# Performance work log

Hardware: AMD Instinct MI355X
Metric: run time of the kernel (lower is better)

## Reference

```python
import jax, jax.numpy as jnp
import numpy as np

L, NH, DH, D, DI, V = 12, 12, 64, 768, 3072, 10000
QLEN, MLEN, CLEN, BSZ = 512, 512, 32, 4
EPS = 1e-5


def _ln(x, g, b):
    m = x.mean(-1, keepdims=True)
    v = ((x - m) ** 2).mean(-1, keepdims=True)
    return (x - m) / jnp.sqrt(v + EPS) * g + b


def _rel_shift(x):
    # x: [B, H, qlen, rlen]; Transformer-XL pad/reshape shift trick
    B, H, q, r = x.shape
    xp = jnp.pad(x, ((0, 0), (0, 0), (0, 0), (1, 0)))
    return xp.reshape(B, H, r + 1, q)[:, :, 1:, :].reshape(B, H, q, r)


def _pos_emb(klen):
    # positions klen-1 .. 0 (relative distances), sinusoidal, dim D
    pos = jnp.arange(klen - 1, -1, -1, dtype=jnp.float32)
    inv = 1.0 / (10000.0 ** (jnp.arange(0, D, 2, dtype=jnp.float32) / D))
    s = pos[:, None] * inv[None, :]
    return jnp.concatenate([jnp.sin(s), jnp.cos(s)], axis=-1)  # [klen, D]


def setup_inputs() -> dict:
    key = jax.random.key(0)
    ks = jax.random.split(key, 21)
    init = lambda k, shape: (0.02 * jax.random.normal(k, shape)).astype(jnp.float32)
    return {
        'x': jax.random.randint(ks[0], (QLEN, BSZ), 0, V),
        'condition': init(ks[1], (CLEN, BSZ, D)) * 50.0,
        'mems': init(ks[2], (L, MLEN, BSZ, D)) * 50.0,
        'emb': init(ks[3], (V, D)),
        'qkv_w': init(ks[4], (L, D, 3 * NH * DH)),
        'r_net_w': init(ks[5], (L, D, NH * DH)),
        'o_w': init(ks[6], (L, NH * DH, D)),
        'ln1_g': jnp.ones((L, D), jnp.float32),
        'ln1_b': jnp.zeros((L, D), jnp.float32),
        'w1': init(ks[7], (L, D, DI)),
        'b1': jnp.zeros((L, DI), jnp.float32),
        'w2': init(ks[8], (L, DI, D)),
        'b2': jnp.zeros((L, D), jnp.float32),
        'ln2_g': jnp.ones((L, D), jnp.float32),
        'ln2_b': jnp.zeros((L, D), jnp.float32),
        'r_w_bias': init(ks[9], (NH, DH)),
        'r_r_bias': init(ks[10], (NH, DH)),
        'proj_w': init(ks[11], (D, V)),
        'proj_b': jnp.zeros((V,), jnp.float32),
    }


def reference(x, condition, mems, emb, qkv_w, r_net_w, o_w, ln1_g, ln1_b,
              w1, b1, w2, b2, ln2_g, ln2_b, r_w_bias, r_r_bias, proj_w, proj_b):
    qlen, bsz = x.shape
    klen = CLEN + MLEN + qlen
    h = emb[x] * jnp.sqrt(jnp.float32(D))  # [qlen, B, D] word emb * sqrt(d_model)
    r = _pos_emb(klen)                      # [klen, D]
    scale = 1.0 / jnp.sqrt(jnp.float32(DH))
    # causal mask: query i may attend to keys j <= CLEN + MLEN + i (True = masked)
    mask = jnp.arange(klen)[None, :] > (jnp.arange(qlen)[:, None] + CLEN + MLEN)
    for l in range(L):
        cat = jnp.concatenate([condition, mems[l], h], axis=0)  # [klen, B, D]
        heads = cat @ qkv_w[l]                                   # [klen, B, 3*NH*DH]
        qh, kh, vh = jnp.split(heads, 3, axis=-1)
        qh = qh[-qlen:].reshape(qlen, bsz, NH, DH)
        kh = kh.reshape(klen, bsz, NH, DH)
        vh = vh.reshape(klen, bsz, NH, DH)
        rk = (r @ r_net_w[l]).reshape(klen, NH, DH)
        AC = jnp.einsum('ibnd,jbnd->bnij', qh + r_w_bias, kh)    # content score
        BD = _rel_shift(jnp.einsum('ibnd,jnd->bnij', qh + r_r_bias, rk))  # position score
        score = (AC + BD) * scale
        score = jnp.where(mask[None, None], -jnp.inf, score)
        prob = jax.nn.softmax(score, axis=-1)
        av = jnp.einsum('bnij,jbnd->ibnd', prob, vh).reshape(qlen, bsz, NH * DH)
        h = _ln(h + av @ o_w[l], ln1_g[l], ln1_b[l])             # post-LN attention
        ff = jax.nn.relu(h @ w1[l] + b1[l]) @ w2[l] + b2[l]
        h = _ln(h + ff, ln2_g[l], ln2_b[l])                      # post-LN FFN
    return h @ proj_w + proj_b  # [qlen, B, n_token] logits
```

## Files before the change

### kernel.cpp

```cpp
#include <hip/hip_runtime.h>
#include <stdint.h>

#define NLAYER 12
#define NH 12
#define DH 64
#define DMODEL 768
#define DI 3072
#define NV 10000
#define QLEN 512
#define MLEN 512
#define CLEN 32
#define BSZ 4
#define KLEN (CLEN + MLEN + QLEN)
#define MQ (QLEN * BSZ)
#define MK (KLEN * BSZ)
#define H3 (3 * NH * DH)
#define HD (NH * DH)
#define NG (BSZ * NH)
#define SROW ((size_t)QLEN * KLEN)
#define KPAD_R 1152
#define NPAD_V 10112
#define NGC 24

typedef __bf16 bf16;
typedef __bf16 bf16x8 __attribute__((ext_vector_type(8)));
typedef float f32x4 __attribute__((ext_vector_type(4)));

__device__ __forceinline__ void gload16(const void* g, void* l) {
    __builtin_amdgcn_global_load_lds((const __attribute__((address_space(1))) void*)g,
                                     (__attribute__((address_space(3))) void*)l, 16, 0, 0);
}

__device__ __forceinline__ void split_store(float x, bf16* __restrict__ hp,
                                            bf16* __restrict__ lp, size_t off) {
    bf16 h = (bf16)x;
    hp[off] = h;
    lp[off] = (bf16)(x - (float)h);
}

__device__ __forceinline__ void raster(int& bx, int& by) {
    int gx = gridDim.x, gy = gridDim.y;
    int nwg = gx * gy;
    int wgid = blockIdx.y * gx + blockIdx.x;
    int q = nwg >> 3, r = nwg & 7;
    int xcd = wgid & 7, lin = wgid >> 3;
    int swz = (xcd < r ? xcd * (q + 1) : r * (q + 1) + (xcd - r) * q) + lin;
    int gsz = gx * 4;
    int grp = swz / gsz, rem = swz % gsz;
    int rows = gy - grp * 4;
    if (rows > 4) rows = 4;
    bx = rem / rows;
    by = grp * 4 + rem % rows;
}

__global__ __launch_bounds__(256) void k_embed(const int* __restrict__ x,
                                               const float* __restrict__ emb,
                                               float* __restrict__ h) {
    int idx = blockIdx.x * 256 + threadIdx.x;
    if (idx >= MQ * DMODEL) return;
    int row = idx / DMODEL;
    int d = idx % DMODEL;
    int tok = x[row];
    h[idx] = emb[(size_t)tok * DMODEL + d] * 27.712812921102035f;
}

__global__ __launch_bounds__(256) void k_posemb(bf16* __restrict__ rh, bf16* __restrict__ rl) {
    int idx = blockIdx.x * 256 + threadIdx.x;
    if (idx >= KPAD_R * DMODEL) return;
    int k = idx / DMODEL;
    int d = idx % DMODEL;
    float v = 0.0f;
    if (k < KLEN) {
        int pos = KLEN - 1 - k;
        int j = (d < DMODEL / 2) ? d : d - DMODEL / 2;
        double inv = exp(-((double)(2 * j) / (double)DMODEL) * log(10000.0));
        double s = (double)pos * inv;
        v = (d < DMODEL / 2) ? (float)sin(s) : (float)cos(s);
    }
    split_store(v, rh, rl, (size_t)idx);
}

__global__ __launch_bounds__(256) void k_zpad(bf16* __restrict__ khH, bf16* __restrict__ khL) {
    int idx = blockIdx.x * 256 + threadIdx.x;
    int tot = NG * (KPAD_R - KLEN) * DH;
    if (idx >= tot) return;
    int g = idx / ((KPAD_R - KLEN) * DH);
    int rem = idx % ((KPAD_R - KLEN) * DH);
    int jr = rem / DH, d = rem % DH;
    size_t off = ((size_t)g * KPAD_R + KLEN + jr) * DH + d;
    khH[off] = (bf16)0.0f;
    khL[off] = (bf16)0.0f;
}

__global__ __launch_bounds__(256) void k_concat(const float* __restrict__ cond,
                                                const float* __restrict__ mem_l,
                                                const float* __restrict__ h,
                                                bf16* __restrict__ catH,
                                                bf16* __restrict__ catL) {
    int idx = blockIdx.x * 256 + threadIdx.x;
    if (idx >= MK * DMODEL) return;
    int row = idx / DMODEL;
    int k = row / BSZ;
    float v;
    if (k < CLEN) v = cond[idx];
    else if (k < CLEN + MLEN) v = mem_l[idx - CLEN * BSZ * DMODEL];
    else v = h[idx - (CLEN + MLEN) * BSZ * DMODEL];
    split_store(v, catH, catL, (size_t)idx);
}

__global__ __launch_bounds__(256) void k_wconv(const float* __restrict__ W,
                                               bf16* __restrict__ Bh,
                                               bf16* __restrict__ Bl,
                                               int K, int N) {
    __shared__ float t[32][33];
    int n0 = blockIdx.x * 32, k0 = blockIdx.y * 32;
    int tc = threadIdx.x & 31, tr = threadIdx.x >> 5;
#pragma unroll
    for (int i = 0; i < 32; i += 8) {
        int n = n0 + tc;
        t[tr + i][tc] = (n < N) ? W[(size_t)(k0 + tr + i) * N + n] : 0.0f;
    }
    __syncthreads();
#pragma unroll
    for (int i = 0; i < 32; i += 8) {
        int n = n0 + tr + i;
        int k = k0 + tc;
        float x = t[tc][tr + i];
        size_t off = (size_t)n * K + k;
        bf16 h = (bf16)x;
        Bh[off] = h;
        Bl[off] = (bf16)(x - (float)h);
    }
}

template <int BM, bool BIAS, bool RELU, bool SPLITOUT, int SK>
__global__ __launch_bounds__(256) void k_mgemm(const bf16* __restrict__ Ahi,
                                               const bf16* __restrict__ Alo,
                                               const bf16* __restrict__ Bhi,
                                               const bf16* __restrict__ Blo,
                                               const float* __restrict__ bias,
                                               float* __restrict__ C,
                                               bf16* __restrict__ Chi,
                                               bf16* __restrict__ Clo,
                                               int M, int N, int K, int ldc) {
    constexpr int MI = (BM == 128) ? 4 : 2;
    __shared__ __align__(16) bf16 As[2][BM][32];
    __shared__ __align__(16) bf16 Bs[2][128][32];
    int bx, by;
    raster(bx, by);
    int z = (SK > 1) ? blockIdx.z : 0;
    int kb = K / SK;
    int kbeg = z * kb, kend = kbeg + kb;
    if (SK > 1) C += (size_t)z * M * ldc;
    int tid = threadIdx.x;
    int lane = tid & 63;
    int wave = tid >> 6;
    int bm = by * BM, bn = bx * 128;
    int wr = (wave >> 1) * (BM / 2), wc = (wave & 1) * 64;
    int fr = lane & 15;
    int fk = (lane >> 4) * 8;

    const f32x4 fzero = {0.f, 0.f, 0.f, 0.f};
    f32x4 acc[MI][4];
#pragma unroll
    for (int i = 0; i < MI; i++)
#pragma unroll
        for (int j = 0; j < 4; j++) acc[i][j] = fzero;

    int r0 = tid >> 2, p0 = (tid & 3) * 8;
    int r1 = r0 + 64, p1 = p0;

    for (int k0 = kbeg; k0 < kend; k0 += 32) {
        if (BM == 128) {
            gload16(Ahi + (size_t)(bm + r0) * K + k0 + p0, &As[0][r0][p0]);
            gload16(Ahi + (size_t)(bm + r1) * K + k0 + p1, &As[0][r1 & (BM - 1)][p1]);
            gload16(Alo + (size_t)(bm + r0) * K + k0 + p0, &As[1][r0][p0]);
            gload16(Alo + (size_t)(bm + r1) * K + k0 + p1, &As[1][r1 & (BM - 1)][p1]);
        } else {
            gload16(Ahi + (size_t)(bm + r0) * K + k0 + p0, &As[0][r0 & (BM - 1)][p0]);
            gload16(Alo + (size_t)(bm + r0) * K + k0 + p0, &As[1][r0 & (BM - 1)][p0]);
        }
        gload16(Bhi + (size_t)(bn + r0) * K + k0 + p0, &Bs[0][r0][p0]);
        gload16(Bhi + (size_t)(bn + r1) * K + k0 + p1, &Bs[0][r1][p1]);
        gload16(Blo + (size_t)(bn + r0) * K + k0 + p0, &Bs[1][r0][p0]);
        gload16(Blo + (size_t)(bn + r1) * K + k0 + p1, &Bs[1][r1][p1]);
        __syncthreads();

        bf16x8 ah[MI], al[MI], bh[4], bl[4];
#pragma unroll
        for (int mi = 0; mi < MI; mi++) {
            ah[mi] = *(const bf16x8*)&As[0][wr + mi * 16 + fr][fk];
            al[mi] = *(const bf16x8*)&As[1][wr + mi * 16 + fr][fk];
        }
#pragma unroll
        for (int ni = 0; ni < 4; ni++) {
            bh[ni] = *(const bf16x8*)&Bs[0][wc + ni * 16 + fr][fk];
            bl[ni] = *(const bf16x8*)&Bs[1][wc + ni * 16 + fr][fk];
        }
#pragma unroll
        for (int mi = 0; mi < MI; mi++)
#pragma unroll
            for (int ni = 0; ni < 4; ni++) {
                acc[mi][ni] = __builtin_amdgcn_mfma_f32_16x16x32_bf16(ah[mi], bh[ni], acc[mi][ni], 0, 0, 0);
                acc[mi][ni] = __builtin_amdgcn_mfma_f32_16x16x32_bf16(ah[mi], bl[ni], acc[mi][ni], 0, 0, 0);
                acc[mi][ni] = __builtin_amdgcn_mfma_f32_16x16x32_bf16(al[mi], bh[ni], acc[mi][ni], 0, 0, 0);
            }
        __syncthreads();
    }

#pragma unroll
    for (int mi = 0; mi < MI; mi++) {
        int rowb = bm + wr + mi * 16 + (lane >> 4) * 4;
#pragma unroll
        for (int ni = 0; ni < 4; ni++) {
            int col = bn + wc + ni * 16 + fr;
            if (col >= N) continue;
            float bv = (BIAS && z == 0) ? bias[col] : 0.0f;
#pragma unroll
            for (int r = 0; r < 4; r++) {
                int row = rowb + r;
                if (row >= M) continue;
                float xv = acc[mi][ni][r] + bv;
                if (RELU) xv = fmaxf(xv, 0.0f);
                size_t off = (size_t)row * ldc + col;
                if (SPLITOUT) {
                    bf16 hh = (bf16)xv;
                    Chi[off] = hh;
                    Clo[off] = (bf16)(xv - (float)hh);
                } else {
                    C[off] = xv;
                }
            }
        }
    }
}

template <int MODE>
__global__ __launch_bounds__(256) void k_mgemm_qkv(const bf16* __restrict__ Ahi,
                                                   const bf16* __restrict__ Alo,
                                                   const bf16* __restrict__ Bhi,
                                                   const bf16* __restrict__ Blo,
                                                   const float* __restrict__ rwb,
                                                   const float* __restrict__ rrb,
                                                   bf16* __restrict__ P0H, bf16* __restrict__ P0L,
                                                   bf16* __restrict__ P1H, bf16* __restrict__ P1L) {
    constexpr int K = DMODEL;
    __shared__ __align__(16) bf16 As[2][128][32];
    __shared__ __align__(16) bf16 Bs[2][128][32];
    int bx, by;
    raster(bx, by);
    int tid = threadIdx.x;
    int lane = tid & 63;
    int wave = tid >> 6;
    int bm = by * 128, bn = bx * 128;
    int wr = (wave >> 1) * 64, wc = (wave & 1) * 64;
    int fr = lane & 15;
    int fk = (lane >> 4) * 8;

    const f32x4 fzero = {0.f, 0.f, 0.f, 0.f};
    f32x4 acc[4][4];
#pragma unroll
    for (int i = 0; i < 4; i++)
#pragma unroll
        for (int j = 0; j < 4; j++) acc[i][j] = fzero;

    int r0 = tid >> 2, p0 = (tid & 3) * 8;
    int r1 = r0 + 64, p1 = p0;

    for (int k0 = 0; k0 < K; k0 += 32) {
        gload16(Ahi + (size_t)(bm + r0) * K + k0 + p0, &As[0][r0][p0]);
        gload16(Ahi + (size_t)(bm + r1) * K + k0 + p1, &As[0][r1][p1]);
        gload16(Alo + (size_t)(bm + r0) * K + k0 + p0, &As[1][r0][p0]);
        gload16(Alo + (size_t)(bm + r1) * K + k0 + p1, &As[1][r1][p1]);
        gload16(Bhi + (size_t)(bn + r0) * K + k0 + p0, &Bs[0][r0][p0]);
        gload16(Bhi + (size_t)(bn + r1) * K + k0 + p1, &Bs[0][r1][p1]);
        gload16(Blo + (size_t)(bn + r0) * K + k0 + p0, &Bs[1][r0][p0]);
        gload16(Blo + (size_t)(bn + r1) * K + k0 + p1, &Bs[1][r1][p1]);
        __syncthreads();

        bf16x8 ah[4], al[4], bh[4], bl[4];
#pragma unroll
        for (int mi = 0; mi < 4; mi++) {
            ah[mi] = *(const bf16x8*)&As[0][wr + mi * 16 + fr][fk];
            al[mi] = *(const bf16x8*)&As[1][wr + mi * 16 + fr][fk];
        }
#pragma unroll
        for (int ni = 0; ni < 4; ni++) {
            bh[ni] = *(const bf16x8*)&Bs[0][wc + ni * 16 + fr][fk];
            bl[ni] = *(const bf16x8*)&Bs[1][wc + ni * 16 + fr][fk];
        }
#pragma unroll
        for (int mi = 0; mi < 4; mi++)
#pragma unroll
            for (int ni = 0; ni < 4; ni++) {
                acc[mi][ni] = __builtin_amdgcn_mfma_f32_16x16x32_bf16(ah[mi], bh[ni], acc[mi][ni], 0, 0, 0);
                acc[mi][ni] = __builtin_amdgcn_mfma_f32_16x16x32_bf16(ah[mi], bl[ni], acc[mi][ni], 0, 0, 0);
                acc[mi][ni] = __builtin_amdgcn_mfma_f32_16x16x32_bf16(al[mi], bh[ni], acc[mi][ni], 0, 0, 0);
            }
        __syncthreads();
    }

#pragma unroll
    for (int mi = 0; mi < 4; mi++) {
        int rowb = bm + wr + mi * 16 + (lane >> 4) * 4;
#pragma unroll
        for (int ni = 0; ni < 4; ni++) {
            int col = bn + wc + ni * 16 + fr;
#pragma unroll
            for (int r = 0; r < 4; r++) {
                int row = rowb + r;
                float xv = acc[mi][ni][r];
                int b = row & 3;
                if (MODE == 0) {
                    int i = row >> 2;
                    int g = b * NH + (col >> 6);
                    int d = col & 63;
                    size_t off = ((size_t)g * QLEN + i) * DH + d;
                    split_store((xv + rwb[col]) * 0.125f, P0H, P0L, off);
                    split_store((xv + rrb[col]) * 0.125f, P1H, P1L, off);
                } else {
                    int j = row >> 2;
                    if (col < HD) {
                        int g = b * NH + (col >> 6);
                        int d = col & 63;
                        split_store(xv, P0H, P0L, ((size_t)g * KPAD_R + j) * DH + d);
                    } else {
                        int c2 = col - HD;
                        int g = b * NH + (c2 >> 6);
                        int d = c2 & 63;
                        split_store(xv, P1H, P1L, ((size_t)g * KLEN + j) * DH + d);
                    }
                }
            }
        }
    }
}

__global__ __launch_bounds__(256) void k_vtconv_b(const bf16* __restrict__ vH,
                                                  const bf16* __restrict__ vL,
                                                  bf16* __restrict__ vtH,
                                                  bf16* __restrict__ vtL,
                                                  int g0) {
    __shared__ bf16 th[32][33], tl[32][33];
    int gl = blockIdx.z;
    int g = g0 + gl;
    int j0 = blockIdx.x * 32, d0 = blockIdx.y * 32;
    int tc = threadIdx.x & 31, tr = threadIdx.x >> 5;
#pragma unroll
    for (int i = 0; i < 32; i += 8) {
        size_t src = ((size_t)g * KLEN + j0 + tr + i) * DH + d0 + tc;
        th[tr + i][tc] = vH[src];
        tl[tr + i][tc] = vL[src];
    }
    __syncthreads();
#pragma unroll
    for (int i = 0; i < 32; i += 8) {
        size_t dst = ((size_t)gl * DH + d0 + tr + i) * KLEN + j0 + tc;
        vtH[dst] = th[tc][tr + i];
        vtL[dst] = tl[tc][tr + i];
    }
}

template <bool SHIFT>
__global__ __launch_bounds__(256) void k_score(const bf16* __restrict__ QH,
                                               const bf16* __restrict__ QL,
                                               const bf16* __restrict__ KHp,
                                               const bf16* __restrict__ KLp,
                                               float* __restrict__ sAc,
                                               int g0) {
    int bm = blockIdx.y * 128, bn = blockIdx.x * 128;
    if (!SHIFT && bn >= bm + 672) return;
    if (SHIFT && bn + bm < 257) return;
    int gl = blockIdx.z;
    int g = g0 + gl;
    int n = g % NH;
    const bf16* Ah = QH + (size_t)g * QLEN * DH;
    const bf16* Al = QL + (size_t)g * QLEN * DH;
    const bf16 *Bh, *Bl;
    int ldb;
    if (SHIFT) { Bh = KHp + n * DH; Bl = KLp + n * DH; ldb = HD; }
    else { Bh = KHp + (size_t)g * KPAD_R * DH; Bl = KLp + (size_t)g * KPAD_R * DH; ldb = DH; }
    float* C = sAc + (size_t)gl * SROW;

    __shared__ __align__(16) bf16 As[2][128][32];
    __shared__ __align__(16) bf16 Bs[2][128][32];
    int tid = threadIdx.x;
    int lane = tid & 63;
    int wave = tid >> 6;
    int wr = (wave >> 1) * 64, wc = (wave & 1) * 64;
    int fr = lane & 15;
    int fk = (lane >> 4) * 8;

    const f32x4 fzero = {0.f, 0.f, 0.f, 0.f};
    f32x4 acc[4][4];
#pragma unroll
    for (int i = 0; i < 4; i++)
#pragma unroll
        for (int j = 0; j < 4; j++) acc[i][j] = fzero;

    int r0 = tid >> 2, p0 = (tid & 3) * 8;
    int r1 = r0 + 64, p1 = p0;

#pragma unroll
    for (int k0 = 0; k0 < DH; k0 += 32) {
        gload16(Ah + (size_t)(bm + r0) * DH + k0 + p0, &As[0][r0][p0]);
        gload16(Ah + (size_t)(bm + r1) * DH + k0 + p1, &As[0][r1][p1]);
        gload16(Al + (size_t)(bm + r0) * DH + k0 + p0, &As[1][r0][p0]);
        gload16(Al + (size_t)(bm + r1) * DH + k0 + p1, &As[1][r1][p1]);
        gload16(Bh + (size_t)(bn + r0) * ldb + k0 + p0, &Bs[0][r0][p0]);
        gload16(Bh + (size_t)(bn + r1) * ldb + k0 + p1, &Bs[0][r1][p1]);
        gload16(Bl + (size_t)(bn + r0) * ldb + k0 + p0, &Bs[1][r0][p0]);
        gload16(Bl + (size_t)(bn + r1) * ldb + k0 + p1, &Bs[1][r1][p1]);
        __syncthreads();

        bf16x8 ah[4], al[4], bh[4], bl[4];
#pragma unroll
        for (int mi = 0; mi < 4; mi++) {
            ah[mi] = *(const bf16x8*)&As[0][wr + mi * 16 + fr][fk];
            al[mi] = *(const bf16x8*)&As[1][wr + mi * 16 + fr][fk];
        }
#pragma unroll
        for (int ni = 0; ni < 4; ni++) {
            bh[ni] = *(const bf16x8*)&Bs[0][wc + ni * 16 + fr][fk];
            bl[ni] = *(const bf16x8*)&Bs[1][wc + ni * 16 + fr][fk];
        }
#pragma unroll
        for (int mi = 0; mi < 4; mi++)
#pragma unroll
            for (int ni = 0; ni < 4; ni++) {
                acc[mi][ni] = __builtin_amdgcn_mfma_f32_16x16x32_bf16(ah[mi], bh[ni], acc[mi][ni], 0, 0, 0);
                acc[mi][ni] = __builtin_amdgcn_mfma_f32_16x16x32_bf16(ah[mi], bl[ni], acc[mi][ni], 0, 0, 0);
                acc[mi][ni] = __builtin_amdgcn_mfma_f32_16x16x32_bf16(al[mi], bh[ni], acc[mi][ni], 0, 0, 0);
            }
        __syncthreads();
    }

#pragma unroll
    for (int mi = 0; mi < 4; mi++) {
        int rowb = bm + wr + mi * 16 + (lane >> 4) * 4;
#pragma unroll
        for (int ni = 0; ni < 4; ni++) {
            int t = bn + wc + ni * 16 + fr;
            if (t >= KLEN) continue;
#pragma unroll
            for (int r = 0; r < 4; r++) {
                int i = rowb + r;
                if (SHIFT) {
                    int j = t - (QLEN - 1) + i;
                    if (j >= 0) C[(size_t)i * KLEN + j] += acc[mi][ni][r];
                } else {
                    C[(size_t)i * KLEN + t] = acc[mi][ni][r];
                }
            }
        }
    }
}

__global__ __launch_bounds__(256) void k_softmax_p(const float* __restrict__ sAc,
                                                   bf16* __restrict__ P) {
    __shared__ float red[256];
    int i = blockIdx.x;
    int gl = blockIdx.y;
    int tid = threadIdx.x;
    const float* row = sAc + (size_t)gl * SROW + (size_t)i * KLEN;
    bf16* pr = P + (size_t)gl * SROW + (size_t)i * KLEN;
    int len = i + CLEN + MLEN + 1;
    float v[5];
    int cnt = 0;
    float mx = -1e30f;
    for (int j = tid; j < len; j += 256) {
        float s = row[j];
        v[cnt++] = s;
        mx = fmaxf(mx, s);
    }
    red[tid] = mx;
    __syncthreads();
    for (int st = 128; st > 0; st >>= 1) {
        if (tid < st) red[tid] = fmaxf(red[tid], red[tid + st]);
        __syncthreads();
    }
    float smax = red[0];
    __syncthreads();
    float sum = 0.f;
    cnt = 0;
    for (int j = tid; j < len; j += 256) {
        float e = __expf(v[cnt] - smax);
        v[cnt] = e;
        sum += e;
        cnt++;
    }
    red[tid] = sum;
    __syncthreads();
    for (int st = 128; st > 0; st >>= 1) {
        if (tid < st) red[tid] += red[tid + st];
        __syncthreads();
    }
    float inv = 1.0f / red[0];
    cnt = 0;
    for (int j = tid; j < len; j += 256) pr[j] = (bf16)(v[cnt++] * inv);
    for (int j = tid; j < KLEN; j += 256)
        if (j >= len) pr[j] = (bf16)0.0f;
}

__global__ __launch_bounds__(256) void k_av(const bf16* __restrict__ P,
                                            const bf16* __restrict__ VH,
                                            const bf16* __restrict__ VL,
                                            bf16* __restrict__ atH,
                                            bf16* __restrict__ atL,
                                            int g0) {
    int gl = blockIdx.z;
    int g = g0 + gl;
    int b = g / NH, n = g % NH;
    const bf16* Ap = P + (size_t)gl * SROW;
    const bf16* Vh = VH + (size_t)gl * DH * KLEN;
    const bf16* Vl = VL + (size_t)gl * DH * KLEN;
    __shared__ __align__(16) bf16 As[64][32];
    __shared__ __align__(16) bf16 Bs[2][64][32];
    int tid = threadIdx.x;
    int lane = tid & 63;
    int wave = tid >> 6;
    int bm = blockIdx.y * 64;
    int fr = lane & 15;
    int fk = (lane >> 4) * 8;
    const f32x4 fzero = {0.f, 0.f, 0.f, 0.f};
    f32x4 acc[4] = {fzero, fzero, fzero, fzero};
    int ra = tid >> 2, pa = (tid & 3) * 8;
    int kmax = bm + 608;
    if (kmax > KLEN) kmax = KLEN;

    for (int k0 = 0; k0 < kmax; k0 += 32) {
        gload16(Ap + (size_t)(bm + ra) * KLEN + k0 + pa, &As[ra][pa]);
        gload16(Vh + (size_t)ra * KLEN + k0 + pa, &Bs[0][ra][pa]);
        gload16(Vl + (size_t)ra * KLEN + k0 + pa, &Bs[1][ra][pa]);
        __syncthreads();
        bf16x8 a = *(const bf16x8*)&As[wave * 16 + fr][fk];
#pragma unroll
        for (int ni = 0; ni < 4; ni++) {
            bf16x8 bh = *(const bf16x8*)&Bs[0][ni * 16 + fr][fk];
            bf16x8 bl = *(const bf16x8*)&Bs[1][ni * 16 + fr][fk];
            acc[ni] = __builtin_amdgcn_mfma_f32_16x16x32_bf16(a, bh, acc[ni], 0, 0, 0);
            acc[ni] = __builtin_amdgcn_mfma_f32_16x16x32_bf16(a, bl, acc[ni], 0, 0, 0);
        }
        __syncthreads();
    }

#pragma unroll
    for (int ni = 0; ni < 4; ni++) {
        int d = ni * 16 + fr;
#pragma unroll
        for (int r = 0; r < 4; r++) {
            int i = bm + wave * 16 + (lane >> 4) * 4 + r;
            size_t off = (size_t)(i * BSZ + b) * HD + n * DH + d;
            split_store(acc[ni][r], atH, atL, off);
        }
    }
}

__global__ __launch_bounds__(256) void k_add_ln(float* __restrict__ h,
                                                const float* __restrict__ d0,
                                                const float* __restrict__ d1,
                                                const float* __restrict__ g,
                                                const float* __restrict__ bta,
                                                bf16* __restrict__ hH,
                                                bf16* __restrict__ hL) {
    __shared__ float xs[DMODEL];
    __shared__ float red[256];
    int row = blockIdx.x;
    int tid = threadIdx.x;
    float* hr = h + (size_t)row * DMODEL;
    const float* dr0 = d0 + (size_t)row * DMODEL;
    const float* dr1 = d1 + (size_t)row * DMODEL;
    float s = 0.f;
    for (int d = tid; d < DMODEL; d += 256) {
        float v = hr[d] + dr0[d] + dr1[d];
        xs[d] = v;
        s += v;
    }
    red[tid] = s;
    __syncthreads();
    for (int st = 128; st > 0; st >>= 1) {
        if (tid < st) red[tid] += red[tid + st];
        __syncthreads();
    }
    float mean = red[0] * (1.0f / DMODEL);
    __syncthreads();
    float v2 = 0.f;
    for (int d = tid; d < DMODEL; d += 256) {
        float t = xs[d] - mean;
        v2 += t * t;
    }
    red[tid] = v2;
    __syncthreads();
    for (int st = 128; st > 0; st >>= 1) {
        if (tid < st) red[tid] += red[tid + st];
        __syncthreads();
    }
    float inv = rsqrtf(red[0] * (1.0f / DMODEL) + 1e-5f);
    for (int d = tid; d < DMODEL; d += 256) {
        float y = (xs[d] - mean) * inv * g[d] + bta[d];
        hr[d] = y;
        split_store(y, hH, hL, (size_t)row * DMODEL + d);
    }
}

extern "C" void kernel_launch(void* const* d_in, const int* in_sizes, int n_in,
                              void* d_out, int out_size, void* d_ws, size_t ws_size,
                              hipStream_t stream) {
    const int* x = (const int*)d_in[0];
    const float* condition = (const float*)d_in[1];
    const float* mems = (const float*)d_in[2];
    const float* emb = (const float*)d_in[3];
    const float* qkv_w = (const float*)d_in[4];
    const float* r_net_w = (const float*)d_in[5];
    const float* o_w = (const float*)d_in[6];
    const float* ln1_g = (const float*)d_in[7];
    const float* ln1_b = (const float*)d_in[8];
    const float* w1 = (const float*)d_in[9];
    const float* b1 = (const float*)d_in[10];
    const float* w2 = (const float*)d_in[11];
    const float* b2 = (const float*)d_in[12];
    const float* ln2_g = (const float*)d_in[13];
    const float* ln2_b = (const float*)d_in[14];
    const float* r_w_bias = (const float*)d_in[15];
    const float* r_r_bias = (const float*)d_in[16];
    const float* proj_w = (const float*)d_in[17];
    const float* proj_b = (const float*)d_in[18];
    float* out = (float*)d_out;

    float* ws = (float*)d_ws;
    float* h = ws;
    float* delta = h + (size_t)MQ * DMODEL;
    float* delta2 = delta + (size_t)MQ * DMODEL;

    bf16* pb = (bf16*)(delta2 + (size_t)MQ * DMODEL);
    bf16* rbH = pb; pb += (size_t)KPAD_R * DMODEL;
    bf16* rbL = pb; pb += (size_t)KPAD_R * DMODEL;
    bf16* rkH = pb; pb += (size_t)KPAD_R * DMODEL;
    bf16* rkL = pb; pb += (size_t)KPAD_R * DMODEL;
    bf16* atH = pb; pb += (size_t)MQ * HD;
    bf16* atL = pb; pb += (size_t)MQ * HD;
    bf16* qwH = pb; pb += (size_t)NG * QLEN * DH;
    bf16* qwL = pb; pb += (size_t)NG * QLEN * DH;
    bf16* qrH = pb; pb += (size_t)NG * QLEN * DH;
    bf16* qrL = pb; pb += (size_t)NG * QLEN * DH;
    bf16* khH = pb; pb += (size_t)NG * KPAD_R * DH;
    bf16* khL = pb; pb += (size_t)NG * KPAD_R * DH;
    bf16* vH_ = pb; pb += (size_t)NG * KLEN * DH;
    bf16* vL_ = pb; pb += (size_t)NG * KLEN * DH;

    bf16* R = pb;
    bf16* BtH = R;
    bf16* BtL = BtH + (size_t)NPAD_V * DMODEL;
    bf16* ffnH = BtL + (size_t)NPAD_V * DMODEL;
    bf16* ffnL = ffnH + (size_t)MQ * DI;
    bf16* catH = ffnL + (size_t)MQ * DI;
    bf16* catL = catH + (size_t)MK * DMODEL;
    bf16* hH = catL + (size_t)MK * DMODEL;
    bf16* hL = hH + (size_t)MQ * DMODEL;

    float* sAc = (float*)R;
    bf16* Pc = (bf16*)(sAc + (size_t)NGC * SROW);
    bf16* vtH = Pc + (size_t)NGC * SROW;
    bf16* vtL = vtH + (size_t)NGC * DH * KLEN;

    dim3 blk(256);
    k_embed<<<dim3((MQ * DMODEL + 255) / 256), blk, 0, stream>>>(x, emb, h);
    k_posemb<<<dim3((KPAD_R * DMODEL + 255) / 256), blk, 0, stream>>>(rbH, rbL);
    k_zpad<<<dim3((NG * (KPAD_R - KLEN) * DH + 255) / 256), blk, 0, stream>>>(khH, khL);

    for (int l = 0; l < NLAYER; l++) {
        k_concat<<<dim3((MK * DMODEL + 255) / 256), blk, 0, stream>>>(
            condition, mems + (size_t)l * MLEN * BSZ * DMODEL, h, catH, catL);

        k_wconv<<<dim3(H3 / 32, DMODEL / 32), blk, 0, stream>>>(
            qkv_w + (size_t)l * DMODEL * H3, BtH, BtL, DMODEL, H3);
        k_mgemm_qkv<1><<<dim3((2 * HD) / 128, MK / 128), blk, 0, stream>>>(
            catH, catL, BtH + (size_t)HD * DMODEL, BtL + (size_t)HD * DMODEL,
            nullptr, nullptr, khH, khL, vH_, vL_);
        k_mgemm_qkv<0><<<dim3(HD / 128, MQ / 128), blk, 0, stream>>>(
            catH + (size_t)(CLEN + MLEN) * BSZ * DMODEL, catL + (size_t)(CLEN + MLEN) * BSZ * DMODEL,
            BtH, BtL, r_w_bias, r_r_bias, qwH, qwL, qrH, qrL);

        k_wconv<<<dim3(HD / 32, DMODEL / 32), blk, 0, stream>>>(
            r_net_w + (size_t)l * DMODEL * HD, BtH, BtL, DMODEL, HD);
        k_mgemm<64, false, false, true, 1><<<dim3(HD / 128, KPAD_R / 64), blk, 0, stream>>>(
            rbH, rbL, BtH, BtL, nullptr, nullptr, rkH, rkL, KPAD_R, HD, DMODEL, HD);

        for (int g0 = 0; g0 < NG; g0 += NGC) {
            k_vtconv_b<<<dim3(KLEN / 32, DH / 32, NGC), blk, 0, stream>>>(vH_, vL_, vtH, vtL, g0);
            k_score<false><<<dim3(KPAD_R / 128, QLEN / 128, NGC), blk, 0, stream>>>(
                qwH, qwL, khH, khL, sAc, g0);
            k_score<true><<<dim3(KPAD_R / 128, QLEN / 128, NGC), blk, 0, stream>>>(
                qrH, qrL, rkH, rkL, sAc, g0);
            k_softmax_p<<<dim3(QLEN, NGC), blk, 0, stream>>>(sAc, Pc);
            k_av<<<dim3(1, QLEN / 64, NGC), blk, 0, stream>>>(Pc, vtH, vtL, atH, atL, g0);
        }

        k_wconv<<<dim3(DMODEL / 32, HD / 32), blk, 0, stream>>>(
            o_w + (size_t)l * HD * DMODEL, BtH, BtL, HD, DMODEL);
        k_mgemm<64, false, false, false, 2><<<dim3(DMODEL / 128, MQ / 64, 2), blk, 0, stream>>>(
            atH, atL, BtH, BtL, nullptr, delta, nullptr, nullptr, MQ, DMODEL, HD, DMODEL);

        k_add_ln<<<dim3(MQ), blk, 0, stream>>>(h, delta, delta2, ln1_g + (size_t)l * DMODEL,
                                               ln1_b + (size_t)l * DMODEL, hH, hL);

        k_wconv<<<dim3(DI / 32, DMODEL / 32), blk, 0, stream>>>(
            w1 + (size_t)l * DMODEL * DI, BtH, BtL, DMODEL, DI);
        k_mgemm<128, true, true, true, 1><<<dim3(DI / 128, MQ / 128), blk, 0, stream>>>(
            hH, hL, BtH, BtL, b1 + (size_t)l * DI, nullptr, ffnH, ffnL, MQ, DI, DMODEL, DI);

        k_wconv<<<dim3(DMODEL / 32, DI / 32), blk, 0, stream>>>(
            w2 + (size_t)l * DI * DMODEL, BtH, BtL, DI, DMODEL);
        k_mgemm<64, true, false, false, 2><<<dim3(DMODEL / 128, MQ / 64, 2), blk, 0, stream>>>(
            ffnH, ffnL, BtH, BtL, b2 + (size_t)l * DMODEL, delta, nullptr, nullptr,
            MQ, DMODEL, DI, DMODEL);

        k_add_ln<<<dim3(MQ), blk, 0, stream>>>(h, delta, delta2, ln2_g + (size_t)l * DMODEL,
                                               ln2_b + (size_t)l * DMODEL, hH, hL);
    }

    k_wconv<<<dim3(NPAD_V / 32, DMODEL / 32), blk, 0, stream>>>(proj_w, BtH, BtL, DMODEL, NV);
    k_mgemm<128, true, false, false, 1><<<dim3(NPAD_V / 128, MQ / 128), blk, 0, stream>>>(
        hH, hL, BtH, BtL, proj_b, out, nullptr, nullptr, MQ, NV, DMODEL, NV);
}
```

Before: 6.509 ms.

## Fuse content score, softmax and AV into a flash-style attention kernel

Replaces the separate content-score GEMM, softmax and P·V kernels with a single online-softmax kernel that computes Q·K per tile, adds a precomputed unshifted position-score matrix read with shifted indexing, and accumulates P·V in registers. The position scores are now written unshifted, with no read-modify-write into a shared score buffer. This removes the float score round-trip and the bf16 probability matrix in global memory. In exchange it adds gathered loads of the position scores and swizzled LDS tiles, and the softmax is rescaled per tile with probabilities rounded to bf16.

```diff
diff --git a/kernel.cpp b/kernel.cpp
--- a/kernel.cpp
+++ b/kernel.cpp
@@ -361,26 +361,22 @@
     }
 }
 
-template <bool SHIFT>
-__global__ __launch_bounds__(256) void k_score(const bf16* __restrict__ QH,
-                                               const bf16* __restrict__ QL,
-                                               const bf16* __restrict__ KHp,
-                                               const bf16* __restrict__ KLp,
-                                               float* __restrict__ sAc,
-                                               int g0) {
+__global__ __launch_bounds__(256) void k_bdt(const bf16* __restrict__ QH,
+                                             const bf16* __restrict__ QL,
+                                             const bf16* __restrict__ RH,
+                                             const bf16* __restrict__ RL,
+                                             float* __restrict__ BDt,
+                                             int g0) {
     int bm = blockIdx.y * 128, bn = blockIdx.x * 128;
-    if (!SHIFT && bn >= bm + 672) return;
-    if (SHIFT && bn + bm < 257) return;
+    if (bn + bm <= 256) return;
     int gl = blockIdx.z;
     int g = g0 + gl;
     int n = g % NH;
     const bf16* Ah = QH + (size_t)g * QLEN * DH;
     const bf16* Al = QL + (size_t)g * QLEN * DH;
-    const bf16 *Bh, *Bl;
-    int ldb;
-    if (SHIFT) { Bh = KHp + n * DH; Bl = KLp + n * DH; ldb = HD; }
-    else { Bh = KHp + (size_t)g * KPAD_R * DH; Bl = KLp + (size_t)g * KPAD_R * DH; ldb = DH; }
-    float* C = sAc + (size_t)gl * SROW;
+    const bf16* Bh = RH + n * DH;
+    const bf16* Bl = RL + n * DH;
+    float* C = BDt + (size_t)gl * SROW;
 
     __shared__ __align__(16) bf16 As[2][128][32];
     __shared__ __align__(16) bf16 Bs[2][128][32];
@@ -407,10 +403,10 @@
         gload16(Ah + (size_t)(bm + r1) * DH + k0 + p1, &As[0][r1][p1]);
         gload16(Al + (size_t)(bm + r0) * DH + k0 + p0, &As[1][r0][p0]);
         gload16(Al + (size_t)(bm + r1) * DH + k0 + p1, &As[1][r1][p1]);
-        gload16(Bh + (size_t)(bn + r0) * ldb + k0 + p0, &Bs[0][r0][p0]);
-        gload16(Bh + (size_t)(bn + r1) * ldb + k0 + p1, &Bs[0][r1][p1]);
-        gload16(Bl + (size_t)(bn + r0) * ldb + k0 + p0, &Bs[1][r0][p0]);
-        gload16(Bl + (size_t)(bn + r1) * ldb + k0 + p1, &Bs[1][r1][p1]);
+        gload16(Bh + (size_t)(bn + r0) * HD + k0 + p0, &Bs[0][r0][p0]);
+        gload16(Bh + (size_t)(bn + r1) * HD + k0 + p1, &Bs[0][r1][p1]);
+        gload16(Bl + (size_t)(bn + r0) * HD + k0 + p0, &Bs[1][r0][p0]);
+        gload16(Bl + (size_t)(bn + r1) * HD + k0 + p1, &Bs[1][r1][p1]);
         __syncthreads();
 
         bf16x8 ah[4], al[4], bh[4], bl[4];
@@ -445,113 +441,186 @@
 #pragma unroll
             for (int r = 0; r < 4; r++) {
                 int i = rowb + r;
-                if (SHIFT) {
-                    int j = t - (QLEN - 1) + i;
-                    if (j >= 0) C[(size_t)i * KLEN + j] += acc[mi][ni][r];
-                } else {
-                    C[(size_t)i * KLEN + t] = acc[mi][ni][r];
-                }
-            }
-        }
-    }
-}
-
-__global__ __launch_bounds__(256) void k_softmax_p(const float* __restrict__ sAc,
-                                                   bf16* __restrict__ P) {
-    __shared__ float red[256];
-    int i = blockIdx.x;
+                C[(size_t)i * KLEN + t] = acc[mi][ni][r];
+            }
+        }
+    }
+}
+
+__global__ __launch_bounds__(256) void k_flash(const bf16* __restrict__ qwH, const bf16* __restrict__ qwL,
+                                               const bf16* __restrict__ khH, const bf16* __restrict__ khL,
+                                               const bf16* __restrict__ vtH, const bf16* __restrict__ vtL,
+                                               const float* __restrict__ BDt,
+                                               bf16* __restrict__ atH, bf16* __restrict__ atL,
+                                               int g0) {
+    __shared__ __align__(16) bf16 LQ[2][64][64];
+    __shared__ __align__(16) bf16 LK[2][64][64];
+    __shared__ __align__(16) bf16 LV[2][64][64];
+    __shared__ __align__(16) bf16 LP[64][64];
     int gl = blockIdx.y;
-    int tid = threadIdx.x;
-    const float* row = sAc + (size_t)gl * SROW + (size_t)i * KLEN;
-    bf16* pr = P + (size_t)gl * SROW + (size_t)i * KLEN;
-    int len = i + CLEN + MLEN + 1;
-    float v[5];
-    int cnt = 0;
-    float mx = -1e30f;
-    for (int j = tid; j < len; j += 256) {
-        float s = row[j];
-        v[cnt++] = s;
-        mx = fmaxf(mx, s);
-    }
-    red[tid] = mx;
-    __syncthreads();
-    for (int st = 128; st > 0; st >>= 1) {
-        if (tid < st) red[tid] = fmaxf(red[tid], red[tid + st]);
-        __syncthreads();
-    }
-    float smax = red[0];
-    __syncthreads();
-    float sum = 0.f;
-    cnt = 0;
-    for (int j = tid; j < len; j += 256) {
-        float e = __expf(v[cnt] - smax);
-        v[cnt] = e;
-        sum += e;
-        cnt++;
-    }
-    red[tid] = sum;
-    __syncthreads();
-    for (int st = 128; st > 0; st >>= 1) {
-        if (tid < st) red[tid] += red[tid + st];
-        __syncthreads();
-    }
-    float inv = 1.0f / red[0];
-    cnt = 0;
-    for (int j = tid; j < len; j += 256) pr[j] = (bf16)(v[cnt++] * inv);
-    for (int j = tid; j < KLEN; j += 256)
-        if (j >= len) pr[j] = (bf16)0.0f;
-}
-
-__global__ __launch_bounds__(256) void k_av(const bf16* __restrict__ P,
-                                            const bf16* __restrict__ VH,
-                                            const bf16* __restrict__ VL,
-                                            bf16* __restrict__ atH,
-                                            bf16* __restrict__ atL,
-                                            int g0) {
-    int gl = blockIdx.z;
     int g = g0 + gl;
     int b = g / NH, n = g % NH;
-    const bf16* Ap = P + (size_t)gl * SROW;
-    const bf16* Vh = VH + (size_t)gl * DH * KLEN;
-    const bf16* Vl = VL + (size_t)gl * DH * KLEN;
-    __shared__ __align__(16) bf16 As[64][32];
-    __shared__ __align__(16) bf16 Bs[2][64][32];
-    int tid = threadIdx.x;
-    int lane = tid & 63;
-    int wave = tid >> 6;
-    int bm = blockIdx.y * 64;
-    int fr = lane & 15;
-    int fk = (lane >> 4) * 8;
-    const f32x4 fzero = {0.f, 0.f, 0.f, 0.f};
-    f32x4 acc[4] = {fzero, fzero, fzero, fzero};
-    int ra = tid >> 2, pa = (tid & 3) * 8;
-    int kmax = bm + 608;
-    if (kmax > KLEN) kmax = KLEN;
-
-    for (int k0 = 0; k0 < kmax; k0 += 32) {
-        gload16(Ap + (size_t)(bm + ra) * KLEN + k0 + pa, &As[ra][pa]);
-        gload16(Vh + (size_t)ra * KLEN + k0 + pa, &Bs[0][ra][pa]);
-        gload16(Vl + (size_t)ra * KLEN + k0 + pa, &Bs[1][ra][pa]);
-        __syncthreads();
-        bf16x8 a = *(const bf16x8*)&As[wave * 16 + fr][fk];
+    int i0 = blockIdx.x * 64;
+    int tid = threadIdx.x, lane = tid & 63, w = tid >> 6;
+    int fr = lane & 15, fq = lane >> 4, fk = fq * 8;
+
+    {
+        const bf16* q0 = qwH + ((size_t)g * QLEN + i0) * DH;
+        const bf16* q1 = qwL + ((size_t)g * QLEN + i0) * DH;
+        int c0 = tid, c1 = tid + 256;
+        gload16(q0 + (c0 >> 3) * DH + (c0 & 7) * 8, &LQ[0][c0 >> 3][(c0 & 7) * 8]);
+        gload16(q0 + (c1 >> 3) * DH + (c1 & 7) * 8, &LQ[0][c1 >> 3][(c1 & 7) * 8]);
+        gload16(q1 + (c0 >> 3) * DH + (c0 & 7) * 8, &LQ[1][c0 >> 3][(c0 & 7) * 8]);
+        gload16(q1 + (c1 >> 3) * DH + (c1 & 7) * 8, &LQ[1][c1 >> 3][(c1 & 7) * 8]);
+    }
+    __syncthreads();
+    bf16x8 aqh[2], aql[2];
+    aqh[0] = *(const bf16x8*)&LQ[0][w * 16 + fr][fk];
+    aqh[1] = *(const bf16x8*)&LQ[0][w * 16 + fr][32 + fk];
+    aql[0] = *(const bf16x8*)&LQ[1][w * 16 + fr][fk];
+    aql[1] = *(const bf16x8*)&LQ[1][w * 16 + fr][32 + fk];
+
+    const f32x4 fz = {0.f, 0.f, 0.f, 0.f};
+    f32x4 ao[4] = {fz, fz, fz, fz};
+    float m[4] = {-3e38f, -3e38f, -3e38f, -3e38f};
+    float l[4] = {0.f, 0.f, 0.f, 0.f};
+
+    const bf16* kb0 = khH + (size_t)g * KPAD_R * DH;
+    const bf16* kb1 = khL + (size_t)g * KPAD_R * DH;
+    const bf16* vb0 = vtH + (size_t)gl * DH * KLEN;
+    const bf16* vb1 = vtL + (size_t)gl * DH * KLEN;
+    const float* bdp = BDt + (size_t)gl * SROW;
+
+    int ntiles = (i0 + 607) / 64 + 1;
+    for (int jt = 0; jt < ntiles; jt++) {
+        int j0 = jt * 64;
+        {
+            int c0 = tid, c1 = tid + 256;
+            int r0 = c0 >> 3, cb0 = (c0 & 7) * 16, s0 = (cb0 ^ ((r0 & 7) << 4)) >> 1;
+            int r1 = c1 >> 3, cb1 = (c1 & 7) * 16, s1 = (cb1 ^ ((r1 & 7) << 4)) >> 1;
+            gload16(kb0 + (size_t)(j0 + r0) * DH + s0, &LK[0][r0][cb0 >> 1]);
+            gload16(kb0 + (size_t)(j0 + r1) * DH + s1, &LK[0][r1][cb1 >> 1]);
+            gload16(kb1 + (size_t)(j0 + r0) * DH + s0, &LK[1][r0][cb0 >> 1]);
+            gload16(kb1 + (size_t)(j0 + r1) * DH + s1, &LK[1][r1][cb1 >> 1]);
+            gload16(vb0 + (size_t)r0 * KLEN + j0 + s0, &LV[0][r0][cb0 >> 1]);
+            gload16(vb0 + (size_t)r1 * KLEN + j0 + s1, &LV[0][r1][cb1 >> 1]);
+            gload16(vb1 + (size_t)r0 * KLEN + j0 + s0, &LV[1][r0][cb0 >> 1]);
+            gload16(vb1 + (size_t)r1 * KLEN + j0 + s1, &LV[1][r1][cb1 >> 1]);
+        }
+        float bd[4][4];
 #pragma unroll
         for (int ni = 0; ni < 4; ni++) {
-            bf16x8 bh = *(const bf16x8*)&Bs[0][ni * 16 + fr][fk];
-            bf16x8 bl = *(const bf16x8*)&Bs[1][ni * 16 + fr][fk];
-            acc[ni] = __builtin_amdgcn_mfma_f32_16x16x32_bf16(a, bh, acc[ni], 0, 0, 0);
-            acc[ni] = __builtin_amdgcn_mfma_f32_16x16x32_bf16(a, bl, acc[ni], 0, 0, 0);
-        }
-        __syncthreads();
-    }
-
-#pragma unroll
-    for (int ni = 0; ni < 4; ni++) {
-        int d = ni * 16 + fr;
+            int j = j0 + ni * 16 + fr;
+#pragma unroll
+            for (int r = 0; r < 4; r++) {
+                int i = i0 + w * 16 + fq * 4 + r;
+                int t = j + (QLEN - 1) - i;
+                if (t > KLEN - 1) t = KLEN - 1;
+                bd[ni][r] = bdp[(size_t)i * KLEN + t];
+            }
+        }
+        __syncthreads();
+        f32x4 sa[4] = {fz, fz, fz, fz};
+#pragma unroll
+        for (int k0 = 0; k0 < 2; k0++) {
+#pragma unroll
+            for (int ni = 0; ni < 4; ni++) {
+                int row = ni * 16 + fr;
+                int cb = ((k0 * 32 + fk) * 2) ^ ((row & 7) << 4);
+                bf16x8 bh = *(const bf16x8*)((const char*)LK[0] + row * 128 + cb);
+                bf16x8 bl = *(const bf16x8*)((const char*)LK[1] + row * 128 + cb);
+                sa[ni] = __builtin_amdgcn_mfma_f32_16x16x32_bf16(aqh[k0], bh, sa[ni], 0, 0, 0);
+                sa[ni] = __builtin_amdgcn_mfma_f32_16x16x32_bf16(aqh[k0], bl, sa[ni], 0, 0, 0);
+                sa[ni] = __builtin_amdgcn_mfma_f32_16x16x32_bf16(aql[k0], bh, sa[ni], 0, 0, 0);
+            }
+        }
+        float mx[4] = {-3e38f, -3e38f, -3e38f, -3e38f};
+        float pe[4][4];
+#pragma unroll
+        for (int ni = 0; ni < 4; ni++) {
+            int j = j0 + ni * 16 + fr;
+#pragma unroll
+            for (int r = 0; r < 4; r++) {
+                int i = i0 + w * 16 + fq * 4 + r;
+                float s = sa[ni][r] + bd[ni][r];
+                s = (j - i <= CLEN + MLEN && j < KLEN) ? s : -1e30f;
+                pe[ni][r] = s;
+                mx[r] = fmaxf(mx[r], s);
+            }
+        }
+#pragma unroll
+        for (int off = 1; off < 16; off <<= 1) {
+#pragma unroll
+            for (int r = 0; r < 4; r++) mx[r] = fmaxf(mx[r], __shfl_xor(mx[r], off, 16));
+        }
+        float al[4], rs[4];
 #pragma unroll
         for (int r = 0; r < 4; r++) {
-            int i = bm + wave * 16 + (lane >> 4) * 4 + r;
+            float mn = fmaxf(m[r], mx[r]);
+            al[r] = __expf(m[r] - mn);
+            m[r] = mn;
+            rs[r] = 0.f;
+        }
+#pragma unroll
+        for (int ni = 0; ni < 4; ni++)
+#pragma unroll
+            for (int r = 0; r < 4; r++) {
+                float e = __expf(pe[ni][r] - m[r]);
+                pe[ni][r] = e;
+                rs[r] += e;
+            }
+#pragma unroll
+        for (int off = 1; off < 16; off <<= 1) {
+#pragma unroll
+            for (int r = 0; r < 4; r++) rs[r] += __shfl_xor(rs[r], off, 16);
+        }
+        f32x4 av;
+#pragma unroll
+        for (int r = 0; r < 4; r++) {
+            l[r] = l[r] * al[r] + rs[r];
+            av[r] = al[r];
+        }
+#pragma unroll
+        for (int d0 = 0; d0 < 4; d0++) ao[d0] *= av;
+#pragma unroll
+        for (int ni = 0; ni < 4; ni++)
+#pragma unroll
+            for (int r = 0; r < 4; r++) {
+                int row = w * 16 + fq * 4 + r;
+                int byt = row * 128 + (((ni * 16 + fr) * 2) ^ ((row & 7) << 4));
+                *(bf16*)((char*)LP + byt) = (bf16)pe[ni][r];
+            }
+        asm volatile("s_waitcnt lgkmcnt(0)" ::: "memory");
+        __builtin_amdgcn_sched_barrier(0);
+#pragma unroll
+        for (int k0 = 0; k0 < 2; k0++) {
+            int prow = w * 16 + fr;
+            int pb = prow * 128 + (((k0 * 32 + fk) * 2) ^ ((prow & 7) << 4));
+            bf16x8 pa = *(const bf16x8*)((const char*)LP + pb);
+#pragma unroll
+            for (int d0 = 0; d0 < 4; d0++) {
+                int vrow = d0 * 16 + fr;
+                int vbyt = vrow * 128 + (((k0 * 32 + fk) * 2) ^ ((vrow & 7) << 4));
+                bf16x8 vh = *(const bf16x8*)((const char*)LV[0] + vbyt);
+                bf16x8 vl = *(const bf16x8*)((const char*)LV[1] + vbyt);
+                ao[d0] = __builtin_amdgcn_mfma_f32_16x16x32_bf16(pa, vh, ao[d0], 0, 0, 0);
+                ao[d0] = __builtin_amdgcn_mfma_f32_16x16x32_bf16(pa, vl, ao[d0], 0, 0, 0);
+            }
+        }
+        __syncthreads();
+    }
+    f32x4 iv;
+#pragma unroll
+    for (int r = 0; r < 4; r++) iv[r] = 1.0f / l[r];
+#pragma unroll
+    for (int d0 = 0; d0 < 4; d0++) {
+        ao[d0] *= iv;
+#pragma unroll
+        for (int r = 0; r < 4; r++) {
+            int i = i0 + w * 16 + fq * 4 + r;
+            int d = d0 * 16 + fr;
             size_t off = (size_t)(i * BSZ + b) * HD + n * DH + d;
-            split_store(acc[ni][r], atH, atL, off);
+            split_store(ao[d0][r], atH, atL, off);
         }
     }
 }
@@ -657,10 +726,8 @@
     bf16* catL = catH + (size_t)MK * DMODEL;
     bf16* hH = catL + (size_t)MK * DMODEL;
     bf16* hL = hH + (size_t)MQ * DMODEL;
-
-    float* sAc = (float*)R;
-    bf16* Pc = (bf16*)(sAc + (size_t)NGC * SROW);
-    bf16* vtH = Pc + (size_t)NGC * SROW;
+    float* BDt = (float*)R;
+    bf16* vtH = (bf16*)(BDt + (size_t)NGC * SROW);
     bf16* vtL = vtH + (size_t)NGC * DH * KLEN;
 
     dim3 blk(256);
@@ -688,12 +755,10 @@
 
         for (int g0 = 0; g0 < NG; g0 += NGC) {
             k_vtconv_b<<<dim3(KLEN / 32, DH / 32, NGC), blk, 0, stream>>>(vH_, vL_, vtH, vtL, g0);
-            k_score<false><<<dim3(KPAD_R / 128, QLEN / 128, NGC), blk, 0, stream>>>(
-                qwH, qwL, khH, khL, sAc, g0);
-            k_score<true><<<dim3(KPAD_R / 128, QLEN / 128, NGC), blk, 0, stream>>>(
-                qrH, qrL, rkH, rkL, sAc, g0);
-            k_softmax_p<<<dim3(QLEN, NGC), blk, 0, stream>>>(sAc, Pc);
-            k_av<<<dim3(1, QLEN / 64, NGC), blk, 0, stream>>>(Pc, vtH, vtL, atH, atL, g0);
+            k_bdt<<<dim3(KPAD_R / 128, QLEN / 128, NGC), blk, 0, stream>>>(
+                qrH, qrL, rkH, rkL, BDt, g0);
+            k_flash<<<dim3(QLEN / 64, NGC), blk, 0, stream>>>(
+                qwH, qwL, khH, khL, vtH, vtL, BDt, atH, atL, g0);
         }
 
         k_wconv<<<dim3(DMODEL / 32, HD / 32), blk, 0, stream>>>(
```

Measured after the change: 5.351 ms. 1.22x faster.
